# Kernel optimization log

Measured on AMD Instinct MI355X. Metric: run time of the kernel, lower is better.

Reference implementation:

```python
import jax, jax.numpy as jnp
import numpy as np

N_NODES = 100000
N_EDGES = 1600000
IN_CH, HID_CH, OUT_CH = 128, 64, 32


def setup_inputs() -> dict:
    key = jax.random.key(0)
    k1, k2, k3, k4 = jax.random.split(key, 4)
    x = jax.random.normal(k1, (N_NODES, IN_CH), dtype=jnp.float32)
    edge_index = jax.random.randint(k2, (2, N_EDGES), 0, N_NODES, dtype=jnp.int32)
    # Glorot-ish scaling like PyG's GCNConv init
    W1 = jax.random.normal(k3, (IN_CH, HID_CH), dtype=jnp.float32) / np.sqrt(IN_CH)
    b1 = jnp.zeros((HID_CH,), dtype=jnp.float32)
    W2 = jax.random.normal(k4, (HID_CH, OUT_CH), dtype=jnp.float32) / np.sqrt(HID_CH)
    b2 = jnp.zeros((OUT_CH,), dtype=jnp.float32)
    return {"x": x, "edge_index": edge_index, "W1": W1, "b1": b1, "W2": W2, "b2": b2}


def reference(x, edge_index, W1, b1, W2, b2):
    # PyG GCNConv semantics: add self-loops, symmetric deg^{-1/2} normalization,
    # linear transform, scatter-add aggregation to destination nodes, add bias.
    N = x.shape[0]
    loops = jnp.arange(N, dtype=edge_index.dtype)
    src = jnp.concatenate([edge_index[0], loops])  # [E+N]
    dst = jnp.concatenate([edge_index[1], loops])  # [E+N]

    deg = jax.ops.segment_sum(jnp.ones_like(src, dtype=x.dtype), dst, num_segments=N)
    dis = jnp.where(deg > 0, jax.lax.rsqrt(jnp.maximum(deg, 1.0)), 0.0)  # deg^{-1/2}
    norm = (dis[src] * dis[dst])[:, None]  # [E+N, 1]

    def gcn_conv(h, W, b):
        h = h @ W                                   # [N, C_out]
        msgs = h[src] * norm                        # gather + scale, [E+N, C_out]
        return jax.ops.segment_sum(msgs, dst, num_segments=N) + b

    h = jax.nn.relu(gcn_conv(x, W1, b1))
    # dropout is identity in eval mode (training=False)
    return gcn_conv(h, W2, b2)
```

## Files before the change

### kernel.cpp

```cpp
#include <hip/hip_runtime.h>
#include <hip/hip_bf16.h>

#define IN_CH 128
#define HID_CH 64
#define OUT_CH 32
#define EPB 2048
#define MAXB 512

typedef unsigned short ushort_t;
typedef __attribute__((ext_vector_type(8))) short short8;
typedef __attribute__((ext_vector_type(4))) float float4v;
using half8 = __attribute__((ext_vector_type(8))) _Float16;

static __device__ __forceinline__ ushort_t f2bf(float f) {
    unsigned u = __float_as_uint(f);
    unsigned r = (u + 0x7fff + ((u >> 16) & 1)) >> 16;
    return (ushort_t)r;
}
static __device__ __forceinline__ float bf_lo(unsigned u) { return __uint_as_float(u << 16); }
static __device__ __forceinline__ float bf_hi(unsigned u) { return __uint_as_float(u & 0xffff0000u); }

static __device__ __forceinline__ unsigned f2h2(float lo, float hi) {
    union { _Float16 h[2]; unsigned u; } v;
    v.h[0] = (_Float16)lo;
    v.h[1] = (_Float16)hi;
    return v.u;
}
static __device__ __forceinline__ unsigned pkh(float a, float b) {
    auto p = __builtin_amdgcn_cvt_pkrtz(a, b);
    union { decltype(p) h; unsigned u; } v;
    v.h = p;
    return v.u;
}


__global__ __launch_bounds__(256) void k_partition(const int* __restrict__ src,
                                                   const int* __restrict__ dst,
                                                   int* __restrict__ gcursor,
                                                   unsigned* __restrict__ pairs,
                                                   int E, int nbk, int cap, int PB,
                                                   const float* __restrict__ W1,
                                                   const float* __restrict__ W2,
                                                   unsigned* __restrict__ wsW) {
    __shared__ int lhist[MAXB];
    __shared__ int lbase[MAXB];
    __shared__ int lcur[MAXB];
    const int tid = threadIdx.x;

    if (blockIdx.x >= PB) {
        int s = (blockIdx.x - PB) * 256 + tid;
        if (s < 1024) {
            int lane = s & 63;
            int nt = (s >> 6) & 3;
            int kc = s >> 8;
            int c = nt * 16 + (lane & 15);
            int k0 = kc * 32 + (lane >> 4) * 8;
            unsigned o[4];
#pragma unroll
            for (int d = 0; d < 4; ++d) {
                unsigned lo = f2bf(W1[(k0 + 2 * d) * 64 + c]);
                unsigned hi = f2bf(W1[(k0 + 2 * d + 1) * 64 + c]);
                o[d] = lo | (hi << 16);
            }
            ((uint4*)wsW)[s] = make_uint4(o[0], o[1], o[2], o[3]);
        } else {
            int q = s - 1024;
            int lane = q & 63;
            int f = q >> 6;
            int c = (f & 1) * 16 + (lane & 15);
            int k0 = (f >> 1) * 32 + (lane >> 4) * 8;
            unsigned o[4];
#pragma unroll
            for (int d = 0; d < 4; ++d)
                o[d] = f2h2(W2[(k0 + 2 * d) * 32 + c], W2[(k0 + 2 * d + 1) * 32 + c]);
            ((uint4*)wsW)[1024 + q] = make_uint4(o[0], o[1], o[2], o[3]);
        }
        return;
    }

    for (int b = tid; b < nbk; b += 256) { lhist[b] = 0; lcur[b] = 0; }
    __syncthreads();
    int s[8], d[8];
    const int e0 = blockIdx.x * EPB;
#pragma unroll
    for (int j = 0; j < 8; ++j) {
        int e = e0 + j * 256 + tid;
        if (e < E) {
            s[j] = src[e];
            d[j] = dst[e];
            atomicAdd(&lhist[d[j] >> 8], 1);
        } else {
            d[j] = -1;
        }
    }
    __syncthreads();
    for (int b = tid; b < nbk; b += 256)
        lbase[b] = lhist[b] ? atomicAdd(&gcursor[b], lhist[b]) : 0;
    __syncthreads();
#pragma unroll
    for (int j = 0; j < 8; ++j) {
        if (d[j] >= 0) {
            int b = d[j] >> 8;
            int loc = atomicAdd(&lcur[b], 1);
            int idx = lbase[b] + loc;
            if (idx < cap)
                pairs[(long long)b * cap + idx] = ((unsigned)s[j] << 8) | (unsigned)(d[j] & 255);
        }
    }
}


__global__ __launch_bounds__(256) void k_bucket_build(const unsigned* __restrict__ pairs,
                                                      const int* __restrict__ gcursor,
                                                      int* __restrict__ rowptr,
                                                      int* __restrict__ col,
                                                      float* __restrict__ dis,
                                                      unsigned* __restrict__ h1zero,
                                                      int cap, int N) {
    __shared__ int lc[256];
    __shared__ int ls[256];
    __shared__ int lcur[256];
    const int b = blockIdx.x, tid = threadIdx.x;

    if (b == 0 && tid < 32) h1zero[tid] = 0;

    int ga = min(gcursor[2 * tid], cap);
    int gb = min(gcursor[2 * tid + 1], cap);
    ls[tid] = ga + gb;
    __syncthreads();
    for (int off = 1; off < 256; off <<= 1) {
        int val = (tid >= off) ? ls[tid - off] : 0;
        __syncthreads();
        ls[tid] += val;
        __syncthreads();
    }
    const int p = b >> 1;
    const int base = (p ? ls[p - 1] : 0) + ((b & 1) ? min(gcursor[b - 1], cap) : 0);
    const int total = ls[255];
    __syncthreads();
    if (b == 0 && tid == 0) rowptr[N] = total;

    lc[tid] = 0;
    __syncthreads();
    const int cnt = min(gcursor[b], cap);
    const unsigned* pp = pairs + (long long)b * cap;
    for (int i = tid; i < cnt; i += 256) atomicAdd(&lc[pp[i] & 255], 1);
    __syncthreads();
    const int v = lc[tid];
    ls[tid] = v;
    __syncthreads();
    for (int off = 1; off < 256; off <<= 1) {
        int val = (tid >= off) ? ls[tid - off] : 0;
        __syncthreads();
        ls[tid] += val;
        __syncthreads();
    }
    const int excl = ls[tid] - v;
    const int row = b * 256 + tid;
    if (row < N) {
        rowptr[row] = base + excl;
        dis[row] = rsqrtf((float)(v + 1));
    }
    lcur[tid] = base + excl;
    __syncthreads();
    for (int i = tid; i < cnt; i += 256) {
        unsigned pk = pp[i];
        int pos = atomicAdd(&lcur[pk & 255], 1);
        col[pos] = (int)(pk >> 8);
    }
}


__global__ __launch_bounds__(256) void k_mm1(const float* __restrict__ X,
                                             const unsigned* __restrict__ wsW,
                                             const float* __restrict__ dis,
                                             ushort_t* __restrict__ H,
                                             unsigned* __restrict__ h2zero, int N) {
    const int tid = threadIdx.x;
    if (blockIdx.x == 0 && tid < 16) h2zero[tid] = 0;

    const int wv = tid >> 6, lane = tid & 63;
    const int quad = lane >> 4, n16 = lane & 15;
    const int rowbase = blockIdx.x * 64 + wv * 16;
    const int myrow = rowbase + n16;
    const bool rok = (myrow < N);

    float4v acc0 = {}, acc1 = {}, acc2 = {}, acc3 = {};

#pragma unroll
    for (int kc = 0; kc < 4; ++kc) {
        float4 xa = make_float4(0.f, 0.f, 0.f, 0.f), xb = xa;
        if (rok) {
            const float4* p = (const float4*)(X + (long long)myrow * 128 + kc * 32 + quad * 8);
            xa = p[0];
            xb = p[1];
        }
        unsigned pk[4];
        pk[0] = (unsigned)f2bf(xa.x) | ((unsigned)f2bf(xa.y) << 16);
        pk[1] = (unsigned)f2bf(xa.z) | ((unsigned)f2bf(xa.w) << 16);
        pk[2] = (unsigned)f2bf(xb.x) | ((unsigned)f2bf(xb.y) << 16);
        pk[3] = (unsigned)f2bf(xb.z) | ((unsigned)f2bf(xb.w) << 16);
        short8 a;
        a[0] = (short)(pk[0] & 0xffff); a[1] = (short)(pk[0] >> 16);
        a[2] = (short)(pk[1] & 0xffff); a[3] = (short)(pk[1] >> 16);
        a[4] = (short)(pk[2] & 0xffff); a[5] = (short)(pk[2] >> 16);
        a[6] = (short)(pk[3] & 0xffff); a[7] = (short)(pk[3] >> 16);

        const short8* wb = (const short8*)wsW;
        short8 b0 = wb[(kc * 4 + 0) * 64 + lane];
        short8 b1 = wb[(kc * 4 + 1) * 64 + lane];
        short8 b2 = wb[(kc * 4 + 2) * 64 + lane];
        short8 b3 = wb[(kc * 4 + 3) * 64 + lane];

        acc0 = __builtin_amdgcn_mfma_f32_16x16x32_bf16(a, b0, acc0, 0, 0, 0);
        acc1 = __builtin_amdgcn_mfma_f32_16x16x32_bf16(a, b1, acc1, 0, 0, 0);
        acc2 = __builtin_amdgcn_mfma_f32_16x16x32_bf16(a, b2, acc2, 0, 0, 0);
        acc3 = __builtin_amdgcn_mfma_f32_16x16x32_bf16(a, b3, acc3, 0, 0, 0);
    }

#pragma unroll
    for (int i = 0; i < 4; ++i) {
        int row = rowbase + quad * 4 + i;
        if (row < N) {
            float dr = dis[row];
            long long o = (long long)row * 64 + n16;
            H[o]      = f2bf(dr * acc0[i]);
            H[o + 16] = f2bf(dr * acc1[i]);
            H[o + 32] = f2bf(dr * acc2[i]);
            H[o + 48] = f2bf(dr * acc3[i]);
        }
    }
}


__global__ __launch_bounds__(256, 8) void k_agg64_mm2(const unsigned* __restrict__ h,
                                                      const int* __restrict__ rowptr,
                                                      const int* __restrict__ col,
                                                      const float* __restrict__ dis,
                                                      const float* __restrict__ b1,
                                                      const unsigned* __restrict__ wsW2,
                                                      unsigned* __restrict__ h2, int N) {
    __shared__ __align__(16) _Float16 zbl[4][64];
    const int tid = threadIdx.x;
    const int wv = tid >> 6, lane = tid & 63;
    const int t = lane & 15, g = lane >> 4;
    const int q8 = g * 8;
    const float4 bq = ((const float4*)b1)[t];

    const half8* wfh = (const half8*)wsW2;
    const half8 bf00 = wfh[lane];
    const half8 bf01 = wfh[64 + lane];
    const half8 bf10 = wfh[128 + lane];
    const half8 bf11 = wfh[192 + lane];

    ushort_t* H2u = (ushort_t*)h2;
    const uint2* h2w = (const uint2*)h;
    const int wave0 = blockIdx.x * 4 + wv;
    const int nwaves = gridDim.x * 4;

    for (int row = wave0; row < N; row += nwaves) {
        const int start = rowptr[row];
        const int deg = rowptr[row + 1] - start;
        const float dr = dis[row];

        int myCol = N;
        if (lane < deg) myCol = col[start + lane];

        uint2 us = h2w[row * 16 + t];
        float2 a01 = make_float2(0.f, 0.f), a23 = make_float2(0.f, 0.f);
        if (g == 0) {
            a01 = make_float2(bf_lo(us.x), bf_hi(us.x));
            a23 = make_float2(bf_lo(us.y), bf_hi(us.y));
        }

#define GAT64(SLOT)                                                   \
    {                                                                 \
        int s_ = __shfl(myCol, (SLOT));                               \
        uint2 uu = h2w[s_ * 16 + t];                                  \
        a01 += make_float2(bf_lo(uu.x), bf_hi(uu.x));                 \
        a23 += make_float2(bf_lo(uu.y), bf_hi(uu.y));                 \
    }
        const int cnt = min(deg, 64);
        for (int k0 = 0; k0 < cnt; k0 += 32) {
            if (cnt - k0 > 16) {
#pragma unroll
                for (int u = 0; u < 8; ++u) GAT64(k0 + 4 * u + g)
            } else {
#pragma unroll
                for (int u = 0; u < 4; ++u) GAT64(k0 + 4 * u + g)
            }
        }
        for (int j = start + 64 + g; j < start + deg; j += 4) {
            int s_ = col[j];
            uint2 uu = h2w[s_ * 16 + t];
            a01 += make_float2(bf_lo(uu.x), bf_hi(uu.x));
            a23 += make_float2(bf_lo(uu.y), bf_hi(uu.y));
        }
#undef GAT64

        float A0 = a01.x, A1 = a01.y, A2 = a23.x, A3 = a23.y;
        A0 += __shfl_down(A0, 32); A1 += __shfl_down(A1, 32);
        A2 += __shfl_down(A2, 32); A3 += __shfl_down(A3, 32);
        A0 += __shfl_down(A0, 16); A1 += __shfl_down(A1, 16);
        A2 += __shfl_down(A2, 16); A3 += __shfl_down(A3, 16);

        if (lane < 16) {
            float z0 = fmaxf(fmaf(dr, A0, bq.x), 0.f);
            float z1 = fmaxf(fmaf(dr, A1, bq.y), 0.f);
            float z2 = fmaxf(fmaf(dr, A2, bq.z), 0.f);
            float z3 = fmaxf(fmaf(dr, A3, bq.w), 0.f);
            *(uint2*)&zbl[wv][4 * t] = make_uint2(pkh(z0, z1), pkh(z2, z3));
        }
        __builtin_amdgcn_wave_barrier();

        half8 af0 = *(const half8*)&zbl[wv][q8];
        half8 af1 = *(const half8*)&zbl[wv][q8 + 32];

        float4v c0 = {};
        c0 = __builtin_amdgcn_mfma_f32_16x16x32_f16(af0, bf00, c0, 0, 0, 0);
        c0 = __builtin_amdgcn_mfma_f32_16x16x32_f16(af1, bf10, c0, 0, 0, 0);
        float4v c1 = {};
        c1 = __builtin_amdgcn_mfma_f32_16x16x32_f16(af0, bf01, c1, 0, 0, 0);
        c1 = __builtin_amdgcn_mfma_f32_16x16x32_f16(af1, bf11, c1, 0, 0, 0);
        __builtin_amdgcn_wave_barrier();

        float v = (lane < 16) ? c0[0] : c1[0];
        if (lane < 32) H2u[row * 32 + lane] = f2bf(dr * v);
    }
}


__global__ __launch_bounds__(256) void k_agg32(const unsigned* __restrict__ h,
                                               const int* __restrict__ rowptr,
                                               const int* __restrict__ col,
                                               const float* __restrict__ dis,
                                               const float* __restrict__ b,
                                               float* __restrict__ out, int N) {
    const int wave = (blockIdx.x * 256 + threadIdx.x) >> 6;
    const int lane = threadIdx.x & 63;
    if (wave >= N) return;
    const int row = wave;
    const int t = lane & 7, g = lane >> 3;

    const int start = rowptr[row];
    const int deg = rowptr[row + 1] - start;
    const float dr = dis[row];

    int myCol = N;
    if (lane < deg) myCol = col[start + lane];

    const uint2* hw = (const uint2*)h;
    uint2 us = hw[row * 8 + t];
    float2 a01 = make_float2(0.f, 0.f), a23 = make_float2(0.f, 0.f);
    if (g == 0) {
        a01 = make_float2(bf_lo(us.x), bf_hi(us.x));
        a23 = make_float2(bf_lo(us.y), bf_hi(us.y));
    }

#define GAT32(SLOT)                                                   \
    {                                                                 \
        int s_ = __shfl(myCol, (SLOT));                               \
        uint2 uu = hw[s_ * 8 + t];                                    \
        a01 += make_float2(bf_lo(uu.x), bf_hi(uu.x));                 \
        a23 += make_float2(bf_lo(uu.y), bf_hi(uu.y));                 \
    }
    const int cnt = min(deg, 64);
    if (cnt > 32) {
#pragma unroll
        for (int u = 0; u < 8; ++u) GAT32(8 * u + g)
    } else if (cnt > 16) {
#pragma unroll
        for (int u = 0; u < 4; ++u) GAT32(8 * u + g)
    } else {
#pragma unroll
        for (int u = 0; u < 2; ++u) GAT32(8 * u + g)
    }
    for (int j = start + 64 + g; j < start + deg; j += 8) {
        int s_ = col[j];
        uint2 uu = hw[s_ * 8 + t];
        a01 += make_float2(bf_lo(uu.x), bf_hi(uu.x));
        a23 += make_float2(bf_lo(uu.y), bf_hi(uu.y));
    }
#undef GAT32

    float A0 = a01.x, A1 = a01.y, A2 = a23.x, A3 = a23.y;
    A0 += __shfl_down(A0, 32); A1 += __shfl_down(A1, 32);
    A2 += __shfl_down(A2, 32); A3 += __shfl_down(A3, 32);
    A0 += __shfl_down(A0, 16); A1 += __shfl_down(A1, 16);
    A2 += __shfl_down(A2, 16); A3 += __shfl_down(A3, 16);
    A0 += __shfl_down(A0, 8);  A1 += __shfl_down(A1, 8);
    A2 += __shfl_down(A2, 8);  A3 += __shfl_down(A3, 8);

    if (lane < 8) {
        float4 bq = ((const float4*)b)[t];
        float4 o;
        o.x = bq.x + dr * A0;
        o.y = bq.y + dr * A1;
        o.z = bq.z + dr * A2;
        o.w = bq.w + dr * A3;
        ((float4*)out)[(long long)row * 8 + t] = o;
    }
}

extern "C" void kernel_launch(void* const* d_in, const int* in_sizes, int n_in,
                              void* d_out, int out_size, void* d_ws, size_t ws_size,
                              hipStream_t stream) {
    const float* x  = (const float*)d_in[0];
    const int*   ei = (const int*)d_in[1];
    const float* W1 = (const float*)d_in[2];
    const float* b1 = (const float*)d_in[3];
    const float* W2 = (const float*)d_in[4];
    const float* b2 = (const float*)d_in[5];
    float* out = (float*)d_out;

    const int N = in_sizes[0] / IN_CH;
    const int E = in_sizes[1] / 2;
    const int* esrc = ei;
    const int* edst = ei + E;

    int nbk = (N + 255) >> 8;
    if (nbk > MAXB) nbk = MAXB;
    const int per_b = (E + nbk - 1) / nbk;
    const int cap = per_b + per_b / 4 + 256;

    int* rowptr   = (int*)d_ws;
    int* gcursor  = rowptr + (((N + 1) + 15) & ~15);
    unsigned* wsW = (unsigned*)(gcursor + MAXB);
    int* col      = (int*)(wsW + 5120);
    float* dis    = (float*)(col + ((E + 15) & ~15));
    ushort_t* h1  = (ushort_t*)(dis + ((N + 15) & ~15));
    unsigned* scratch = (unsigned*)(h1 + (((long long)(N + 1) * 64 + 31) & ~31LL));
    unsigned* pairs = scratch;
    unsigned* h2    = scratch;

    const int B = 256;
    const int PB = (E + EPB - 1) / EPB;

    hipMemsetAsync(gcursor, 0, MAXB * sizeof(int), stream);
    k_partition<<<PB + 5, B, 0, stream>>>(esrc, edst, gcursor, pairs, E, nbk, cap, PB, W1, W2, wsW);
    k_bucket_build<<<nbk, B, 0, stream>>>(pairs, gcursor, rowptr, col, dis,
                                          (unsigned*)(h1 + (long long)N * 64), cap, N);

    k_mm1<<<(N + 63) / 64, B, 0, stream>>>(x, wsW, dis, h1, h2 + (long long)N * 16, N);

    k_agg64_mm2<<<2048, B, 0, stream>>>((const unsigned*)h1, rowptr, col, dis, b1,
                                        wsW + 4096, h2, N);

    k_agg32<<<(int)(((long long)N * 64 + B - 1) / B), B, 0, stream>>>((const unsigned*)h2, rowptr, col, dis, b2, out, N);
}
```

Measured before the change: 244.9 us.

## Process 8 rows per wave with atomic work stealing in aggregation kernels

Both aggregation kernels now give each wave 8 destination rows, 8 lanes per row. Each lane gathers 16-byte chunks and accumulates its own feature slice, so the cross-lane shuffle reductions are gone. Work is handed out dynamically through a global atomic counter, which k_mm1 initializes, instead of a fixed grid stride. The layer-2 MFMA now covers 8 rows at once, which uses the 16x16 tile better. The cost is lanes left idle on low-degree rows, a serial per-lane loop for degrees above 32, and extra atomics.

```diff
diff --git a/kernel.cpp b/kernel.cpp
--- a/kernel.cpp
+++ b/kernel.cpp
@@ -175,9 +175,11 @@
                                              const unsigned* __restrict__ wsW,
                                              const float* __restrict__ dis,
                                              ushort_t* __restrict__ H,
-                                             unsigned* __restrict__ h2zero, int N) {
+                                             unsigned* __restrict__ h2zero,
+                                             int* __restrict__ wctr, int initv, int N) {
     const int tid = threadIdx.x;
     if (blockIdx.x == 0 && tid < 16) h2zero[tid] = 0;
+    if (blockIdx.x == 0 && tid == 0) { wctr[0] = initv; wctr[1] = initv; }
 
     const int wv = tid >> 6, lane = tid & 63;
     const int quad = lane >> 4, n16 = lane & 15;
@@ -233,19 +235,20 @@
 }
 
 
-__global__ __launch_bounds__(256, 8) void k_agg64_mm2(const unsigned* __restrict__ h,
+__global__ __launch_bounds__(256, 4) void k_agg64_mm2(const unsigned* __restrict__ h,
                                                       const int* __restrict__ rowptr,
                                                       const int* __restrict__ col,
                                                       const float* __restrict__ dis,
                                                       const float* __restrict__ b1,
                                                       const unsigned* __restrict__ wsW2,
-                                                      unsigned* __restrict__ h2, int N) {
-    __shared__ __align__(16) _Float16 zbl[4][64];
+                                                      unsigned* __restrict__ h2,
+                                                      int* __restrict__ wctr, int N) {
+    __shared__ __align__(16) _Float16 zbl[4][8][64];
     const int tid = threadIdx.x;
     const int wv = tid >> 6, lane = tid & 63;
-    const int t = lane & 15, g = lane >> 4;
-    const int q8 = g * 8;
-    const float4 bq = ((const float4*)b1)[t];
+    const int t = lane & 7, g = lane >> 3;
+    const float4 bqa = ((const float4*)b1)[2 * t];
+    const float4 bqb = ((const float4*)b1)[2 * t + 1];
 
     const half8* wfh = (const half8*)wsW2;
     const half8 bf00 = wfh[lane];
@@ -254,151 +257,182 @@
     const half8 bf11 = wfh[192 + lane];
 
     ushort_t* H2u = (ushort_t*)h2;
-    const uint2* h2w = (const uint2*)h;
-    const int wave0 = blockIdx.x * 4 + wv;
-    const int nwaves = gridDim.x * 4;
-
-    for (int row = wave0; row < N; row += nwaves) {
-        const int start = rowptr[row];
-        const int deg = rowptr[row + 1] - start;
-        const float dr = dis[row];
-
-        int myCol = N;
-        if (lane < deg) myCol = col[start + lane];
-
-        uint2 us = h2w[row * 16 + t];
-        float2 a01 = make_float2(0.f, 0.f), a23 = make_float2(0.f, 0.f);
-        if (g == 0) {
-            a01 = make_float2(bf_lo(us.x), bf_hi(us.x));
-            a23 = make_float2(bf_lo(us.y), bf_hi(us.y));
-        }
-
-#define GAT64(SLOT)                                                   \
+    const uint4* h4 = (const uint4*)h;
+    const int NB = (N + 7) >> 3;
+    int rb = blockIdx.x * 4 + wv;
+
+    while (rb < NB) {
+        const int r0 = rb * 8;
+        int rp_l = rowptr[min(r0 + min(lane, 8), N)];
+        float dis_l = (lane < 8 && r0 + lane < N) ? dis[r0 + lane] : 0.f;
+        const int sg = __shfl(rp_l, g);
+        const int dg = __shfl(rp_l, g + 1) - sg;
+        const float drg = __shfl(dis_l, g);
+        float dr03[4];
+#pragma unroll
+        for (int i = 0; i < 4; ++i) dr03[i] = __shfl(dis_l, ((lane >> 4) & 1) * 4 + i);
+
+        int mc1 = N, mc2 = N, mc3 = N;
+        if (t < dg)      mc1 = col[sg + t];
+        if (8 + t < dg)  mc2 = col[sg + 8 + t];
+        if (16 + t < dg) mc3 = col[sg + 16 + t];
+
+        const int rme = min(r0 + g, N);
+        uint4 us = h4[rme * 8 + t];
+        float2 p0 = make_float2(bf_lo(us.x), bf_hi(us.x));
+        float2 p1 = make_float2(bf_lo(us.y), bf_hi(us.y));
+        float2 p2 = make_float2(bf_lo(us.z), bf_hi(us.z));
+        float2 p3 = make_float2(bf_lo(us.w), bf_hi(us.w));
+
+#define GATX(MC, U)                                                   \
     {                                                                 \
-        int s_ = __shfl(myCol, (SLOT));                               \
-        uint2 uu = h2w[s_ * 16 + t];                                  \
-        a01 += make_float2(bf_lo(uu.x), bf_hi(uu.x));                 \
-        a23 += make_float2(bf_lo(uu.y), bf_hi(uu.y));                 \
-    }
-        const int cnt = min(deg, 64);
-        for (int k0 = 0; k0 < cnt; k0 += 32) {
-            if (cnt - k0 > 16) {
-#pragma unroll
-                for (int u = 0; u < 8; ++u) GAT64(k0 + 4 * u + g)
-            } else {
-#pragma unroll
-                for (int u = 0; u < 4; ++u) GAT64(k0 + 4 * u + g)
-            }
-        }
-        for (int j = start + 64 + g; j < start + deg; j += 4) {
-            int s_ = col[j];
-            uint2 uu = h2w[s_ * 16 + t];
-            a01 += make_float2(bf_lo(uu.x), bf_hi(uu.x));
-            a23 += make_float2(bf_lo(uu.y), bf_hi(uu.y));
-        }
-#undef GAT64
-
-        float A0 = a01.x, A1 = a01.y, A2 = a23.x, A3 = a23.y;
-        A0 += __shfl_down(A0, 32); A1 += __shfl_down(A1, 32);
-        A2 += __shfl_down(A2, 32); A3 += __shfl_down(A3, 32);
-        A0 += __shfl_down(A0, 16); A1 += __shfl_down(A1, 16);
-        A2 += __shfl_down(A2, 16); A3 += __shfl_down(A3, 16);
-
-        if (lane < 16) {
-            float z0 = fmaxf(fmaf(dr, A0, bq.x), 0.f);
-            float z1 = fmaxf(fmaf(dr, A1, bq.y), 0.f);
-            float z2 = fmaxf(fmaf(dr, A2, bq.z), 0.f);
-            float z3 = fmaxf(fmaf(dr, A3, bq.w), 0.f);
-            *(uint2*)&zbl[wv][4 * t] = make_uint2(pkh(z0, z1), pkh(z2, z3));
+        int s_ = __shfl((MC), (g << 3) + (U));                        \
+        uint4 uu = h4[s_ * 8 + t];                                    \
+        p0 += make_float2(bf_lo(uu.x), bf_hi(uu.x));                  \
+        p1 += make_float2(bf_lo(uu.y), bf_hi(uu.y));                  \
+        p2 += make_float2(bf_lo(uu.z), bf_hi(uu.z));                  \
+        p3 += make_float2(bf_lo(uu.w), bf_hi(uu.w));                  \
+    }
+#pragma unroll
+        for (int u = 0; u < 8; ++u) GATX(mc1, u)
+#pragma unroll
+        for (int u = 0; u < 8; ++u) GATX(mc2, u)
+#pragma unroll
+        for (int u = 0; u < 8; ++u) GATX(mc3, u)
+        if (__any(dg > 24)) {
+            int mc4 = N;
+            if (24 + t < dg) mc4 = col[sg + 24 + t];
+#pragma unroll
+            for (int u = 0; u < 8; ++u) GATX(mc4, u)
+        }
+        for (int u = 32; u < dg; ++u) {
+            int s_ = col[sg + u];
+            uint4 uu = h4[s_ * 8 + t];
+            p0 += make_float2(bf_lo(uu.x), bf_hi(uu.x));
+            p1 += make_float2(bf_lo(uu.y), bf_hi(uu.y));
+            p2 += make_float2(bf_lo(uu.z), bf_hi(uu.z));
+            p3 += make_float2(bf_lo(uu.w), bf_hi(uu.w));
+        }
+#undef GATX
+
+        {
+            float z0 = fmaxf(fmaf(drg, p0.x, bqa.x), 0.f);
+            float z1 = fmaxf(fmaf(drg, p0.y, bqa.y), 0.f);
+            float z2 = fmaxf(fmaf(drg, p1.x, bqa.z), 0.f);
+            float z3 = fmaxf(fmaf(drg, p1.y, bqa.w), 0.f);
+            float z4 = fmaxf(fmaf(drg, p2.x, bqb.x), 0.f);
+            float z5 = fmaxf(fmaf(drg, p2.y, bqb.y), 0.f);
+            float z6 = fmaxf(fmaf(drg, p3.x, bqb.z), 0.f);
+            float z7 = fmaxf(fmaf(drg, p3.y, bqb.w), 0.f);
+            *(uint4*)&zbl[wv][g][8 * t] =
+                make_uint4(pkh(z0, z1), pkh(z2, z3), pkh(z4, z5), pkh(z6, z7));
         }
         __builtin_amdgcn_wave_barrier();
 
-        half8 af0 = *(const half8*)&zbl[wv][q8];
-        half8 af1 = *(const half8*)&zbl[wv][q8 + 32];
-
-        float4v c0 = {};
+        const int zr = lane & 7;
+        const int ko = (lane >> 4) * 8;
+        half8 af0 = *(const half8*)&zbl[wv][zr][ko];
+        half8 af1 = *(const half8*)&zbl[wv][zr][ko + 32];
+        float4v c0 = {}, c1 = {};
         c0 = __builtin_amdgcn_mfma_f32_16x16x32_f16(af0, bf00, c0, 0, 0, 0);
         c0 = __builtin_amdgcn_mfma_f32_16x16x32_f16(af1, bf10, c0, 0, 0, 0);
-        float4v c1 = {};
         c1 = __builtin_amdgcn_mfma_f32_16x16x32_f16(af0, bf01, c1, 0, 0, 0);
         c1 = __builtin_amdgcn_mfma_f32_16x16x32_f16(af1, bf11, c1, 0, 0, 0);
         __builtin_amdgcn_wave_barrier();
 
-        float v = (lane < 16) ? c0[0] : c1[0];
-        if (lane < 32) H2u[row * 32 + lane] = f2bf(dr * v);
-    }
-}
-
-
-__global__ __launch_bounds__(256) void k_agg32(const unsigned* __restrict__ h,
-                                               const int* __restrict__ rowptr,
-                                               const int* __restrict__ col,
-                                               const float* __restrict__ dis,
-                                               const float* __restrict__ b,
-                                               float* __restrict__ out, int N) {
-    const int wave = (blockIdx.x * 256 + threadIdx.x) >> 6;
-    const int lane = threadIdx.x & 63;
-    if (wave >= N) return;
-    const int row = wave;
+        if (lane < 32) {
+            const int li = lane >> 4;
+            const int cc = lane & 15;
+#pragma unroll
+            for (int i = 0; i < 4; ++i) {
+                int rr = r0 + li * 4 + i;
+                if (rr < N) {
+                    H2u[rr * 32 + cc]      = f2bf(dr03[i] * c0[i]);
+                    H2u[rr * 32 + 16 + cc] = f2bf(dr03[i] * c1[i]);
+                }
+            }
+        }
+
+        int nb = 0;
+        if (lane == 0) nb = atomicAdd(wctr, 1);
+        rb = __shfl(nb, 0);
+    }
+}
+
+
+__global__ __launch_bounds__(256, 4) void k_agg32(const unsigned* __restrict__ h,
+                                                  const int* __restrict__ rowptr,
+                                                  const int* __restrict__ col,
+                                                  const float* __restrict__ dis,
+                                                  const float* __restrict__ b,
+                                                  float* __restrict__ out,
+                                                  int* __restrict__ wctr, int N) {
+    const int tid = threadIdx.x;
+    const int wv = tid >> 6, lane = tid & 63;
     const int t = lane & 7, g = lane >> 3;
-
-    const int start = rowptr[row];
-    const int deg = rowptr[row + 1] - start;
-    const float dr = dis[row];
-
-    int myCol = N;
-    if (lane < deg) myCol = col[start + lane];
-
+    const float4 bq = ((const float4*)b)[t];
     const uint2* hw = (const uint2*)h;
-    uint2 us = hw[row * 8 + t];
-    float2 a01 = make_float2(0.f, 0.f), a23 = make_float2(0.f, 0.f);
-    if (g == 0) {
-        a01 = make_float2(bf_lo(us.x), bf_hi(us.x));
-        a23 = make_float2(bf_lo(us.y), bf_hi(us.y));
-    }
-
-#define GAT32(SLOT)                                                   \
+    const int NB = (N + 7) >> 3;
+    int rb = blockIdx.x * 4 + wv;
+
+    while (rb < NB) {
+        const int r0 = rb * 8;
+        int rp_l = rowptr[min(r0 + min(lane, 8), N)];
+        float dis_l = (lane < 8 && r0 + lane < N) ? dis[r0 + lane] : 0.f;
+        const int sg = __shfl(rp_l, g);
+        const int dg = __shfl(rp_l, g + 1) - sg;
+        const float drg = __shfl(dis_l, g);
+
+        int mc1 = N, mc2 = N, mc3 = N;
+        if (t < dg)      mc1 = col[sg + t];
+        if (8 + t < dg)  mc2 = col[sg + 8 + t];
+        if (16 + t < dg) mc3 = col[sg + 16 + t];
+
+        const int rme = min(r0 + g, N);
+        uint2 us = hw[rme * 8 + t];
+        float2 p0 = make_float2(bf_lo(us.x), bf_hi(us.x));
+        float2 p1 = make_float2(bf_lo(us.y), bf_hi(us.y));
+
+#define GAT2(MC, U)                                                   \
     {                                                                 \
-        int s_ = __shfl(myCol, (SLOT));                               \
+        int s_ = __shfl((MC), (g << 3) + (U));                        \
         uint2 uu = hw[s_ * 8 + t];                                    \
-        a01 += make_float2(bf_lo(uu.x), bf_hi(uu.x));                 \
-        a23 += make_float2(bf_lo(uu.y), bf_hi(uu.y));                 \
-    }
-    const int cnt = min(deg, 64);
-    if (cnt > 32) {
-#pragma unroll
-        for (int u = 0; u < 8; ++u) GAT32(8 * u + g)
-    } else if (cnt > 16) {
-#pragma unroll
-        for (int u = 0; u < 4; ++u) GAT32(8 * u + g)
-    } else {
-#pragma unroll
-        for (int u = 0; u < 2; ++u) GAT32(8 * u + g)
-    }
-    for (int j = start + 64 + g; j < start + deg; j += 8) {
-        int s_ = col[j];
-        uint2 uu = hw[s_ * 8 + t];
-        a01 += make_float2(bf_lo(uu.x), bf_hi(uu.x));
-        a23 += make_float2(bf_lo(uu.y), bf_hi(uu.y));
-    }
-#undef GAT32
-
-    float A0 = a01.x, A1 = a01.y, A2 = a23.x, A3 = a23.y;
-    A0 += __shfl_down(A0, 32); A1 += __shfl_down(A1, 32);
-    A2 += __shfl_down(A2, 32); A3 += __shfl_down(A3, 32);
-    A0 += __shfl_down(A0, 16); A1 += __shfl_down(A1, 16);
-    A2 += __shfl_down(A2, 16); A3 += __shfl_down(A3, 16);
-    A0 += __shfl_down(A0, 8);  A1 += __shfl_down(A1, 8);
-    A2 += __shfl_down(A2, 8);  A3 += __shfl_down(A3, 8);
-
-    if (lane < 8) {
-        float4 bq = ((const float4*)b)[t];
-        float4 o;
-        o.x = bq.x + dr * A0;
-        o.y = bq.y + dr * A1;
-        o.z = bq.z + dr * A2;
-        o.w = bq.w + dr * A3;
-        ((float4*)out)[(long long)row * 8 + t] = o;
+        p0 += make_float2(bf_lo(uu.x), bf_hi(uu.x));                  \
+        p1 += make_float2(bf_lo(uu.y), bf_hi(uu.y));                  \
+    }
+#pragma unroll
+        for (int u = 0; u < 8; ++u) GAT2(mc1, u)
+#pragma unroll
+        for (int u = 0; u < 8; ++u) GAT2(mc2, u)
+#pragma unroll
+        for (int u = 0; u < 8; ++u) GAT2(mc3, u)
+        if (__any(dg > 24)) {
+            int mc4 = N;
+            if (24 + t < dg) mc4 = col[sg + 24 + t];
+#pragma unroll
+            for (int u = 0; u < 8; ++u) GAT2(mc4, u)
+        }
+        for (int u = 32; u < dg; ++u) {
+            int s_ = col[sg + u];
+            uint2 uu = hw[s_ * 8 + t];
+            p0 += make_float2(bf_lo(uu.x), bf_hi(uu.x));
+            p1 += make_float2(bf_lo(uu.y), bf_hi(uu.y));
+        }
+#undef GAT2
+
+        const int rr = r0 + g;
+        if (rr < N) {
+            float4 o;
+            o.x = bq.x + drg * p0.x;
+            o.y = bq.y + drg * p0.y;
+            o.z = bq.z + drg * p1.x;
+            o.w = bq.w + drg * p1.y;
+            ((float4*)out)[(long long)rr * 8 + t] = o;
+        }
+
+        int nb = 0;
+        if (lane == 0) nb = atomicAdd(wctr + 1, 1);
+        rb = __shfl(nb, 0);
     }
 }
 
@@ -425,7 +459,8 @@
 
     int* rowptr   = (int*)d_ws;
     int* gcursor  = rowptr + (((N + 1) + 15) & ~15);
-    unsigned* wsW = (unsigned*)(gcursor + MAXB);
+    int* wctr     = gcursor + MAXB;
+    unsigned* wsW = (unsigned*)(wctr + 16);
     int* col      = (int*)(wsW + 5120);
     float* dis    = (float*)(col + ((E + 15) & ~15));
     ushort_t* h1  = (ushort_t*)(dis + ((N + 15) & ~15));
@@ -435,16 +470,19 @@
 
     const int B = 256;
     const int PB = (E + EPB - 1) / EPB;
+    const int AGG_BLOCKS = 1024;
 
     hipMemsetAsync(gcursor, 0, MAXB * sizeof(int), stream);
     k_partition<<<PB + 5, B, 0, stream>>>(esrc, edst, gcursor, pairs, E, nbk, cap, PB, W1, W2, wsW);
     k_bucket_build<<<nbk, B, 0, stream>>>(pairs, gcursor, rowptr, col, dis,
                                           (unsigned*)(h1 + (long long)N * 64), cap, N);
 
-    k_mm1<<<(N + 63) / 64, B, 0, stream>>>(x, wsW, dis, h1, h2 + (long long)N * 16, N);
-
-    k_agg64_mm2<<<2048, B, 0, stream>>>((const unsigned*)h1, rowptr, col, dis, b1,
-                                        wsW + 4096, h2, N);
-
-    k_agg32<<<(int)(((long long)N * 64 + B - 1) / B), B, 0, stream>>>((const unsigned*)h2, rowptr, col, dis, b2, out, N);
-}
+    k_mm1<<<(N + 63) / 64, B, 0, stream>>>(x, wsW, dis, h1, h2 + (long long)N * 16,
+                                           wctr, AGG_BLOCKS * 4, N);
+
+    k_agg64_mm2<<<AGG_BLOCKS, B, 0, stream>>>((const unsigned*)h1, rowptr, col, dis, b1,
+                                              wsW + 4096, h2, wctr, N);
+
+    k_agg32<<<AGG_BLOCKS, B, 0, stream>>>((const unsigned*)h2, rowptr, col, dis, b2, out,
+                                          wctr, N);
+}
```

New measurement: 459.8 us. +87.8%, slower.
